# Kernel tuning notes

Measured on AMD Instinct MI355X. Metric: run time of the kernel, lower is better.

The kernel has to match this reference:

```python
import jax, jax.numpy as jnp
from jax import lax
import numpy as np

SIGMA = 0.4        # guided-attention diagonal width
PAD_MAG = 1e12     # -inf surrogate used by the torch viterbi


def _viterbi_align(logp, text_lens, mel_lens):
    """Monotonic forced alignment. logp: (B, L, T). Returns hard alignment (B, L, T)."""
    B, L, T = logp.shape
    neg = jnp.asarray(-PAD_MAG, logp.dtype)
    # ---- forward DP over time (lax.scan replaces the python loop over T) ----
    init = jnp.full((B, L), neg, logp.dtype).at[:, 0].set(logp[:, 0, 0])
    lp_T = jnp.moveaxis(logp, 2, 0)  # (T, B, L)

    def fwd(prev, lp_t):
        # transition: stay at same text token, or advance by one (shift down along L)
        shifted = jnp.concatenate([jnp.full((B, 1), neg, logp.dtype), prev[:, :-1]], axis=1)
        cur = jnp.maximum(prev, shifted) + lp_t
        return cur, cur

    _, betas = lax.scan(fwd, init, lp_T[1:])
    log_beta = jnp.concatenate([init[None], betas], axis=0)  # (T, B, L), indexed [t, b, l]

    # ---- backtracking (faithful to the float row/col arithmetic in the source) ----
    barange = jnp.arange(B)
    rows0 = (text_lens - 1).astype(logp.dtype)
    cols0 = (mel_lens - 1).astype(logp.dtype)

    def bwd(carry, _):
        rows, cols = carry
        r = rows.astype(jnp.int32)
        c = cols.astype(jnp.int32)
        cm1 = (c - 1) % T  # torch negative indexing wraps; emulate with mod
        g_go = log_beta[cm1, barange, (r - 1) % L]
        g_stay = log_beta[cm1, barange, r % L]
        is_go = (g_go > g_stay).astype(logp.dtype)
        new_rows = jnp.maximum(rows - is_go + 1.0, 0.0) - 1.0  # relu(x)-1 as in source
        new_cols = jnp.maximum(cols, 0.0) - 1.0
        return (new_rows, new_cols), new_rows

    _, rows_seq = lax.scan(bwd, (rows0, cols0), None, length=T - 1)  # r_1 .. r_{T-1}
    path = jnp.concatenate([rows_seq[::-1], rows0[None]], axis=0).T  # (B, T)

    # one-hot over text positions (static width L instead of path.max()+1)
    align = (path[:, :, None] == jnp.arange(L, dtype=path.dtype)[None, None, :]).astype(logp.dtype)  # (B,T,L)

    # per-batch shift: drop first (T - mel_len) frames, zero-pad at the end
    pad = T - mel_lens  # (B,)
    t_idx = jnp.arange(T)[None, :] + pad[:, None]  # (B, T)
    valid = (t_idx < T)
    gathered = jnp.take_along_axis(align, jnp.clip(t_idx, 0, T - 1)[:, :, None], axis=1)
    align = gathered * valid[:, :, None].astype(logp.dtype)
    return jnp.swapaxes(align, 1, 2)  # (B, L, T)


def _guided_attention_loss(att_ws, ilens, olens, sigma=SIGMA):
    """att_ws: (B, T_out, T_in). Masked guided-attention loss (scalar)."""
    B, T, L = att_ws.shape
    t = jnp.arange(T, dtype=att_ws.dtype)[None, :, None]
    l = jnp.arange(L, dtype=att_ws.dtype)[None, None, :]
    il = ilens.astype(att_ws.dtype)[:, None, None]
    ol = olens.astype(att_ws.dtype)[:, None, None]
    w = 1.0 - jnp.exp(-((l / il - t / ol) ** 2) / (2.0 * sigma * sigma))
    valid = (t < ol) & (l < il)
    return jnp.sum(jnp.where(valid, w * att_ws, 0.0)) / jnp.sum(olens).astype(att_ws.dtype)


def setup_inputs() -> dict:
    key = jax.random.key(0)
    k1, k2, k3, k4 = jax.random.split(key, 4)
    B, L, T = 32, 256, 2048
    log_prob_matrix = jax.nn.log_softmax(jax.random.normal(k1, (B, L, T), jnp.float32), axis=1)
    att_ws = jax.nn.softmax(jax.random.normal(k2, (B, T, L), jnp.float32), axis=-1)
    text_lengths = jax.random.randint(k3, (B,), L // 2, L + 1, dtype=jnp.int32)
    mel_lengths = jax.random.randint(k4, (B,), T // 2, T + 1, dtype=jnp.int32)
    return {
        "log_prob_matrix": log_prob_matrix,
        "att_ws": att_ws,
        "text_lengths": text_lengths,
        "mel_lengths": mel_lengths,
    }


def reference(log_prob_matrix, att_ws, text_lengths, mel_lengths):
    # n_frames_per_step = 1 -> olens = mel_lengths (clamped to att width T, trivially true)
    loss = _guided_attention_loss(att_ws, text_lengths, mel_lengths)
    align = _viterbi_align(log_prob_matrix, text_lengths, mel_lengths)
    return loss, align
```

## Files before the change

### kernel.cpp

```cpp
#include <hip/hip_runtime.h>
#include <cstdint>

#define NEG (-1e12f)
constexpr int Bn = 32, Ln = 256, Tn = 2048;
constexpr int TB = Tn / 64;


__device__ inline float dpp_ror1(float x) {
    int xi = __float_as_int(x);
    return __int_as_float(__builtin_amdgcn_update_dpp(xi, xi, 0x13C, 0xF, 0xF, false));
}

__device__ inline uint32_t lds_off(const void* p) {
    return (uint32_t)(uintptr_t)(__attribute__((address_space(3))) const void*)p;
}

#define BARRIER() { asm volatile("" ::: "memory"); \
                    __builtin_amdgcn_s_barrier(); \
                    asm volatile("" ::: "memory"); }

#define DSRX(DST, ROW, BUF) \
    asm volatile("ds_read_b128 %0, %1 offset:%c2" \
        : "=&v"(DST) \
        : "v"((((ROW) >> 2) & 1) ? vxb : vxa), \
          "i"((BUF) * 16384 + ((ROW) & 15) * 1024));

#define W4 { asm volatile("s_waitcnt lgkmcnt(4)"); __builtin_amdgcn_sched_barrier(0); }

#define ABIT(ACC, X, Y) \
    asm("v_cmp_gt_f32 vcc, %1, %2\n\tv_addc_co_u32 %0, vcc, %0, %0, vcc" \
        : "+v"(ACC) : "v"(X), "v"(Y) : "vcc");

#define STEPS(S, Q) { \
    if ((((S) - 1) & 32) == 0) { ABIT(a0hi, svp, pv0) } else { ABIT(a0lo, svp, pv0) } \
    float c3 = fmaxf(pv3, pv2) + (Q).w; \
    float sv = dpp_ror1(c3); \
    float c2 = fmaxf(pv2, pv1) + (Q).z; \
    float c1 = fmaxf(pv1, pv0) + (Q).y; \
    float lf = isl0 ? negc : svp; \
    float c0 = fmaxf(pv0, lf) + (Q).x; \
    if (((S) & 32) == 0) { \
        ABIT(a1hi, c0, c1) ABIT(a2hi, c1, c2) ABIT(a3hi, c2, c3) \
    } else { \
        ABIT(a1lo, c0, c1) ABIT(a2lo, c1, c2) ABIT(a3lo, c2, c3) \
    } \
    if ((S) == 63) { \
        bb[(size_t)(4 * lane + 1) * TB + m] = ((uint64_t)a1hi << 32) | a1lo; \
        bb[(size_t)(4 * lane + 2) * TB + m] = ((uint64_t)a2hi << 32) | a2lo; \
        bb[(size_t)(4 * lane + 3) * TB + m] = ((uint64_t)a3hi << 32) | a3lo; \
        a1lo = a1hi = a2lo = a2hi = a3lo = a3hi = 0; \
    } \
    if ((S) == 64) { \
        bb[(size_t)(4 * lane + 0) * TB + m] = ((uint64_t)a0hi << 32) | a0lo; \
        a0lo = a0hi = 0; \
    } \
    pv0 = c0; pv1 = c1; pv2 = c2; pv3 = c3; svp = sv; }

#define COMP16X(I) { \
    W4 \
    STEPS(16*(I)+ 1, qq0) STEPS(16*(I)+ 2, qq1) STEPS(16*(I)+ 3, qq2) STEPS(16*(I)+ 4, qq3) \
    DSRX(qq0,  9, (I)) DSRX(qq1, 10, (I)) DSRX(qq2, 11, (I)) DSRX(qq3, 12, (I)) \
    W4 \
    STEPS(16*(I)+ 5, qq4) STEPS(16*(I)+ 6, qq5) STEPS(16*(I)+ 7, qq6) STEPS(16*(I)+ 8, qq7) \
    DSRX(qq4, 13, (I)) DSRX(qq5, 14, (I)) DSRX(qq6, 15, (I)) DSRX(qq7,  0, ((I)+1)&3) \
    W4 \
    STEPS(16*(I)+ 9, qq0) STEPS(16*(I)+10, qq1) STEPS(16*(I)+11, qq2) STEPS(16*(I)+12, qq3) \
    DSRX(qq0,  1, ((I)+1)&3) DSRX(qq1,  2, ((I)+1)&3) DSRX(qq2,  3, ((I)+1)&3) DSRX(qq3,  4, ((I)+1)&3) \
    W4 \
    STEPS(16*(I)+13, qq4) STEPS(16*(I)+14, qq5) STEPS(16*(I)+15, qq6) STEPS(16*(I)+16, qq7) \
    DSRX(qq4,  5, ((I)+1)&3) DSRX(qq5,  6, ((I)+1)&3) DSRX(qq6,  7, ((I)+1)&3) DSRX(qq7,  8, ((I)+1)&3) \
    BARRIER() }

#define PLOAD(P) { \
    xh0 = *(const float4*)(pr0 + 16 * (P)); \
    xh1 = *(const float4*)(pr1 + 16 * (P)); \
    xh2 = *(const float4*)(pr2 + 16 * (P)); \
    xh3 = *(const float4*)(pr3 + 16 * (P)); \
    xh4 = *(const float4*)(pr4 + 16 * (P)); \
    if (six) xh5 = *(const float4*)(pr5 + 16 * (P)); }

#define PW1(XH, CC) { float* rq = rr + (CC); \
    rq[0] = (XH).x; rq[256] = (XH).y; rq[512] = (XH).z; rq[768] = (XH).w; }

#define PWRITE(P) { \
    float* rr = smem + ((P) & 3) * 4096; \
    PW1(xh0, c0) PW1(xh1, c1) PW1(xh2, c2) PW1(xh3, c3) PW1(xh4, c4) \
    if (six) PW1(xh5, c5) }

__global__ void __launch_bounds__(256, 1) k_mega(
        const float* __restrict__ logp, const float* __restrict__ att,
        const int* __restrict__ ilen, const int* __restrict__ olen,
        uint64_t* __restrict__ bits, float* __restrict__ partial) {
    __shared__ __align__(16) float smem[24576];
    int bid = blockIdx.x, tid = threadIdx.x;

    if (bid < 32) {
        int b = bid;
        if (tid < 64) {
            __builtin_amdgcn_s_setprio(1);
            int lane = tid;
            bool isl0 = (lane == 0);
            uint64_t* bb = bits + (size_t)b * (Ln * TB);
            const float negc = NEG;
            uint32_t lb = lds_off(smem) + (uint32_t)(lane * 16);
            uint32_t vxa = lb, vxb = lb ^ 64;

            float pv0, pv1, pv2, pv3, svp;
            uint32_t a0lo = 0, a0hi = 0, a1lo = 0, a1hi = 0;
            uint32_t a2lo = 0, a2hi = 0, a3lo = 0, a3hi = 0;

            {
                float lp00 = logp[(size_t)b * (Ln * Tn)];
                pv0 = isl0 ? lp00 : NEG;
                pv1 = NEG; pv2 = NEG; pv3 = NEG;
                svp = dpp_ror1(pv3);
                a1hi = (pv0 > pv1) ? 1u : 0u;
                a2hi = (pv1 > pv2) ? 1u : 0u;
                a3hi = (pv2 > pv3) ? 1u : 0u;
            }

            BARRIER();
            float4 qq0, qq1, qq2, qq3, qq4, qq5, qq6, qq7;
            DSRX(qq0, 1, 0) DSRX(qq1, 2, 0) DSRX(qq2, 3, 0) DSRX(qq3, 4, 0)
            DSRX(qq4, 5, 0) DSRX(qq5, 6, 0) DSRX(qq6, 7, 0) DSRX(qq7, 8, 0)

            for (int m = 0; m < 32; ++m) {
                COMP16X(0) COMP16X(1) COMP16X(2) COMP16X(3)
            }
            asm volatile("s_waitcnt vmcnt(0)" ::: "memory");
        } else {
            int tid2 = tid - 64;
            bool six = (tid2 < 64);
            const float* lpb = logp + (size_t)b * (Ln * Tn);
            int v0 = tid2, v1 = tid2 + 192, v2 = tid2 + 384,
                v3 = tid2 + 576, v4 = tid2 + 768, v5 = tid2 + 960;
            const float* pr0 = lpb + (size_t)(v0 >> 2) * Tn + 4 * (v0 & 3);
            const float* pr1 = lpb + (size_t)(v1 >> 2) * Tn + 4 * (v1 & 3);
            const float* pr2 = lpb + (size_t)(v2 >> 2) * Tn + 4 * (v2 & 3);
            const float* pr3 = lpb + (size_t)(v3 >> 2) * Tn + 4 * (v3 & 3);
            const float* pr4 = lpb + (size_t)(v4 >> 2) * Tn + 4 * (v4 & 3);
            const float* pr5 = lpb + (size_t)(v5 >> 2) * Tn + 4 * (v5 & 3);
            int c0 = (4 * (v0 & 3)) * 256 + ((v0 >> 2) ^ ((v0 & 1) << 4));
            int c1 = (4 * (v1 & 3)) * 256 + ((v1 >> 2) ^ ((v1 & 1) << 4));
            int c2 = (4 * (v2 & 3)) * 256 + ((v2 >> 2) ^ ((v2 & 1) << 4));
            int c3 = (4 * (v3 & 3)) * 256 + ((v3 >> 2) ^ ((v3 & 1) << 4));
            int c4 = (4 * (v4 & 3)) * 256 + ((v4 >> 2) ^ ((v4 & 1) << 4));
            int c5 = (4 * (v5 & 3)) * 256 + ((v5 >> 2) ^ ((v5 & 1) << 4));
            float4 xh0, xh1, xh2, xh3, xh4, xh5;

            PLOAD(0) PWRITE(0)
            PLOAD(1) PWRITE(1)
            PLOAD(2)
            asm volatile("s_waitcnt lgkmcnt(0)" ::: "memory");
            BARRIER();

            for (int k = 0; k < 128; ++k) {
                if (k <= 125) PWRITE(k + 2)
                if (k <= 124) PLOAD(k + 3)
                asm volatile("s_waitcnt lgkmcnt(0)" ::: "memory");
                BARRIER();
            }
        }
    } else {
        const int N4 = Bn * Tn * Ln / 4;
        int j = bid - 32;
        int idx = j * 256 + tid;
        int stride = 1024 * 256;
        float acc = 0.f;
        for (int v = idx; v < N4; v += stride) {
            int flat = v << 2;
            int b  = flat >> 19;
            int t  = (flat >> 8) & (Tn - 1);
            int l0 = flat & (Ln - 1);
            int ili = ilen[b];
            int oli = olen[b];
            if (t >= oli) continue;
            float il = (float)ili, ol = (float)oli;
            float tf = (float)t / ol;
            float4 a = reinterpret_cast<const float4*>(att)[v];
            #pragma unroll
            for (int c = 0; c < 4; ++c) {
                int l = l0 + c;
                float av = (c == 0) ? a.x : (c == 1) ? a.y : (c == 2) ? a.z : a.w;
                if (l < ili) {
                    float d = (float)l / il - tf;
                    acc += (1.f - __expf(-d * d * 3.125f)) * av;
                }
            }
        }
        for (int off = 32; off > 0; off >>= 1) acc += __shfl_down(acc, off, 64);
        float* sw = smem;
        if ((tid & 63) == 0) sw[tid >> 6] = acc;
        __syncthreads();
        if (tid == 0) partial[j] = (sw[0] + sw[1]) + (sw[2] + sw[3]);
    }
}

__global__ void __launch_bounds__(256) k_backtrack(const uint64_t* __restrict__ bits,
                                                   const int* __restrict__ ilen,
                                                   const int* __restrict__ olen,
                                                   int2* __restrict__ ext) {
    __shared__ uint64_t sb[Ln * TB];
    int b = blockIdx.x, tid = threadIdx.x;
    ext[b * Ln + tid] = make_int2(1, 0);
    const ulonglong2* g = (const ulonglong2*)(bits + (size_t)b * (Ln * TB));
    ulonglong2* s2 = (ulonglong2*)sb;
    #pragma unroll
    for (int i = 0; i < 16; ++i) s2[i * 256 + tid] = g[i * 256 + tid];
    __syncthreads();
    if (tid != 0) return;

    int tl = ilen[b], ml = olen[b];
    int2* eb = ext + b * Ln;
    int r = tl - 1, hi = ml - 1, p = ml - 2;
    if (p < 0) { eb[r] = make_int2(0, hi); return; }
    int c = p >> 6;
    #define LDW(RR) __builtin_bitreverse64(sb[(RR) * TB + c])
    uint64_t w0 = LDW(r);
    uint64_t w1 = LDW(r > 0 ? r - 1 : 0);
    uint64_t w2 = LDW(r > 1 ? r - 2 : 0);
    uint64_t w3 = LDW(r > 2 ? r - 3 : 0);
    int vd = 3;
    while (true) {
        int pb = p & 63;
        uint64_t mask = (pb == 63) ? ~0ull : ((1ull << (pb + 1)) - 1ull);
        uint64_t mm = w0 & mask;
        if (mm == 0) {
            p = (p & ~63) - 1;
            if (p < 0) { eb[r] = make_int2(0, hi); break; }
            c = p >> 6;
            w0 = LDW(r);
            w1 = LDW(r > 0 ? r - 1 : 0);
            w2 = LDW(r > 1 ? r - 2 : 0);
            w3 = LDW(r > 2 ? r - 3 : 0);
            vd = 3;
        } else {
            int q = 63 - __builtin_clzll(mm);
            int tq = (p & ~63) + q;
            eb[r] = make_int2(tq + 1, hi);
            r -= 1;
            if (r < 0) break;
            hi = tq;
            p = tq - 1;
            if (p < 0) { eb[r] = make_int2(0, hi); break; }
            w0 = w1; w1 = w2; w2 = w3; vd -= 1;
            int nc = p >> 6;
            if (nc != c || vd == 0) {
                c = nc;
                w0 = LDW(r);
                w1 = LDW(r > 0 ? r - 1 : 0);
                w2 = LDW(r > 1 ? r - 2 : 0);
                w3 = LDW(r > 2 ? r - 3 : 0);
                vd = 3;
            }
        }
    }
    #undef LDW
}

__global__ void k_fill(const int2* __restrict__ ext, const float* __restrict__ partial,
                       const int* __restrict__ olen, float* __restrict__ out) {
    const int NG = (Bn * Ln * Tn) / 4;
    int idx = blockIdx.x * blockDim.x + threadIdx.x;
    int stride = gridDim.x * blockDim.x;
    for (int i = idx; i < NG; i += stride) {
        if (i == 0) {
            int2 e = ext[0];
            out[1] = (0 >= e.x && 0 <= e.y) ? 1.f : 0.f;
            out[2] = (1 >= e.x && 1 <= e.y) ? 1.f : 0.f;
            out[3] = (2 >= e.x && 2 <= e.y) ? 1.f : 0.f;
            int2 el = ext[Bn * Ln - 1];
            out[(size_t)Bn * Ln * Tn] = (2047 >= el.x && 2047 <= el.y) ? 1.f : 0.f;
            continue;
        }
        int f0 = 4 * i - 1;
        int r0 = f0 >> 11;
        int t0 = f0 & 2047;
        int2 e0 = ext[r0];
        float4 v;
        if (t0 != 2047) {
            v.x = (t0     >= e0.x && t0     <= e0.y) ? 1.f : 0.f;
            v.y = (t0 + 1 >= e0.x && t0 + 1 <= e0.y) ? 1.f : 0.f;
            v.z = (t0 + 2 >= e0.x && t0 + 2 <= e0.y) ? 1.f : 0.f;
            v.w = (t0 + 3 >= e0.x && t0 + 3 <= e0.y) ? 1.f : 0.f;
        } else {
            int2 e1 = ext[r0 + 1];
            v.x = (2047 >= e0.x && 2047 <= e0.y) ? 1.f : 0.f;
            v.y = (0 >= e1.x && 0 <= e1.y) ? 1.f : 0.f;
            v.z = (1 >= e1.x && 1 <= e1.y) ? 1.f : 0.f;
            v.w = (2 >= e1.x && 2 <= e1.y) ? 1.f : 0.f;
        }
        *reinterpret_cast<float4*>(out + (size_t)4 * i) = v;
    }
    if (blockIdx.x == 0) {
        int tid = threadIdx.x;
        float acc = 0.f;
        for (int i = tid; i < 1024; i += 256) acc += partial[i];
        for (int off = 32; off > 0; off >>= 1) acc += __shfl_down(acc, off, 64);
        __shared__ float sw[4];
        if ((tid & 63) == 0) sw[tid >> 6] = acc;
        __syncthreads();
        if (tid == 0) {
            float tot = (sw[0] + sw[1]) + (sw[2] + sw[3]);
            int so = 0;
            for (int i = 0; i < Bn; ++i) so += olen[i];
            out[0] = tot / (float)so;
        }
    }
}

extern "C" void kernel_launch(void* const* d_in, const int* in_sizes, int n_in,
                              void* d_out, int out_size, void* d_ws, size_t ws_size,
                              hipStream_t stream) {
    const float* logp = (const float*)d_in[0];
    const float* att  = (const float*)d_in[1];
    const int* tlen   = (const int*)d_in[2];
    const int* mlen   = (const int*)d_in[3];
    float* out = (float*)d_out;
    uint64_t* bits = (uint64_t*)d_ws;
    float* partial = (float*)((char*)d_ws + 2097152);
    int2* ext = (int2*)((char*)d_ws + 2101248);

    k_mega<<<32 + 1024, 256, 0, stream>>>(logp, att, tlen, mlen, bits, partial);
    k_backtrack<<<Bn, 256, 0, stream>>>(bits, tlen, mlen, ext);
    k_fill<<<2048, 256, 0, stream>>>(ext, partial, mlen, out);
}
```

Before: 135.5 us.

## Zero output in mega kernel, fuse backtrack with sparse one-hot fill

The output is zero-filled by 1024 extra blocks that run concurrently inside the DP/loss mega kernel. The backtrack kernel now keeps its segment extents in LDS and writes only the 1.0 entries of each row, which lets the separate full-output fill kernel and its workspace round-trip be dropped. This is meant to hide the 64MB output write behind the serial Viterbi DP and to remove a launch. The risk is that the zeroing blocks compete for bandwidth with the loss blocks, and the sparse per-row writes are uncoalesced and serialized per thread.

Measured after the change: 130.4 us. 3.7% less time.

```diff
diff --git a/kernel.cpp b/kernel.cpp
--- a/kernel.cpp
+++ b/kernel.cpp
@@ -90,7 +90,8 @@
 __global__ void __launch_bounds__(256, 1) k_mega(
         const float* __restrict__ logp, const float* __restrict__ att,
         const int* __restrict__ ilen, const int* __restrict__ olen,
-        uint64_t* __restrict__ bits, float* __restrict__ partial) {
+        uint64_t* __restrict__ bits, float* __restrict__ partial,
+        float* __restrict__ out) {
     __shared__ __align__(16) float smem[24576];
     int bid = blockIdx.x, tid = threadIdx.x;
 
@@ -161,7 +162,7 @@
                 BARRIER();
             }
         }
-    } else {
+    } else if (bid < 32 + 1024) {
         const int N4 = Bn * Tn * Ln / 4;
         int j = bid - 32;
         int idx = j * 256 + tid;
@@ -193,111 +194,93 @@
         if ((tid & 63) == 0) sw[tid >> 6] = acc;
         __syncthreads();
         if (tid == 0) partial[j] = (sw[0] + sw[1]) + (sw[2] + sw[3]);
+    } else {
+        const int NZ = (Bn * Ln * Tn) / 4;
+        int j = bid - 1056;
+        float4 z = make_float4(0.f, 0.f, 0.f, 0.f);
+        for (int i = j * 256 + tid; i < NZ; i += 1024 * 256)
+            reinterpret_cast<float4*>(out)[i] = z;
+        if (j == 0 && tid == 0) out[(size_t)Bn * Ln * Tn] = 0.f;
     }
 }
 
-__global__ void __launch_bounds__(256) k_backtrack(const uint64_t* __restrict__ bits,
-                                                   const int* __restrict__ ilen,
-                                                   const int* __restrict__ olen,
-                                                   int2* __restrict__ ext) {
+__global__ void __launch_bounds__(256) k_tail(const uint64_t* __restrict__ bits,
+                                              const int* __restrict__ ilen,
+                                              const int* __restrict__ olen,
+                                              const float* __restrict__ partial,
+                                              float* __restrict__ out) {
     __shared__ uint64_t sb[Ln * TB];
+    __shared__ int2 eb[Ln];
+    __shared__ float sw[4];
     int b = blockIdx.x, tid = threadIdx.x;
-    ext[b * Ln + tid] = make_int2(1, 0);
+    eb[tid] = make_int2(1, 0);
     const ulonglong2* g = (const ulonglong2*)(bits + (size_t)b * (Ln * TB));
     ulonglong2* s2 = (ulonglong2*)sb;
     #pragma unroll
     for (int i = 0; i < 16; ++i) s2[i * 256 + tid] = g[i * 256 + tid];
     __syncthreads();
-    if (tid != 0) return;
-
-    int tl = ilen[b], ml = olen[b];
-    int2* eb = ext + b * Ln;
-    int r = tl - 1, hi = ml - 1, p = ml - 2;
-    if (p < 0) { eb[r] = make_int2(0, hi); return; }
-    int c = p >> 6;
-    #define LDW(RR) __builtin_bitreverse64(sb[(RR) * TB + c])
-    uint64_t w0 = LDW(r);
-    uint64_t w1 = LDW(r > 0 ? r - 1 : 0);
-    uint64_t w2 = LDW(r > 1 ? r - 2 : 0);
-    uint64_t w3 = LDW(r > 2 ? r - 3 : 0);
-    int vd = 3;
-    while (true) {
-        int pb = p & 63;
-        uint64_t mask = (pb == 63) ? ~0ull : ((1ull << (pb + 1)) - 1ull);
-        uint64_t mm = w0 & mask;
-        if (mm == 0) {
-            p = (p & ~63) - 1;
-            if (p < 0) { eb[r] = make_int2(0, hi); break; }
-            c = p >> 6;
-            w0 = LDW(r);
-            w1 = LDW(r > 0 ? r - 1 : 0);
-            w2 = LDW(r > 1 ? r - 2 : 0);
-            w3 = LDW(r > 2 ? r - 3 : 0);
-            vd = 3;
-        } else {
-            int q = 63 - __builtin_clzll(mm);
-            int tq = (p & ~63) + q;
-            eb[r] = make_int2(tq + 1, hi);
-            r -= 1;
-            if (r < 0) break;
-            hi = tq;
-            p = tq - 1;
-            if (p < 0) { eb[r] = make_int2(0, hi); break; }
-            w0 = w1; w1 = w2; w2 = w3; vd -= 1;
-            int nc = p >> 6;
-            if (nc != c || vd == 0) {
-                c = nc;
-                w0 = LDW(r);
-                w1 = LDW(r > 0 ? r - 1 : 0);
-                w2 = LDW(r > 1 ? r - 2 : 0);
-                w3 = LDW(r > 2 ? r - 3 : 0);
-                vd = 3;
-            }
+
+    if (tid == 0) {
+        int tl = ilen[b], ml = olen[b];
+        int r = tl - 1, hi = ml - 1, p = ml - 2;
+        if (p < 0) { eb[r] = make_int2(0, hi); }
+        else {
+            int c = p >> 6;
+            #define LDW(RR) __builtin_bitreverse64(sb[(RR) * TB + c])
+            uint64_t w0 = LDW(r);
+            uint64_t w1 = LDW(r > 0 ? r - 1 : 0);
+            uint64_t w2 = LDW(r > 1 ? r - 2 : 0);
+            uint64_t w3 = LDW(r > 2 ? r - 3 : 0);
+            int vd = 3;
+            while (true) {
+                int pb = p & 63;
+                uint64_t mask = (pb == 63) ? ~0ull : ((1ull << (pb + 1)) - 1ull);
+                uint64_t mm = w0 & mask;
+                if (mm == 0) {
+                    p = (p & ~63) - 1;
+                    if (p < 0) { eb[r] = make_int2(0, hi); break; }
+                    c = p >> 6;
+                    w0 = LDW(r);
+                    w1 = LDW(r > 0 ? r - 1 : 0);
+                    w2 = LDW(r > 1 ? r - 2 : 0);
+                    w3 = LDW(r > 2 ? r - 3 : 0);
+                    vd = 3;
+                } else {
+                    int q = 63 - __builtin_clzll(mm);
+                    int tq = (p & ~63) + q;
+                    eb[r] = make_int2(tq + 1, hi);
+                    r -= 1;
+                    if (r < 0) break;
+                    hi = tq;
+                    p = tq - 1;
+                    if (p < 0) { eb[r] = make_int2(0, hi); break; }
+                    w0 = w1; w1 = w2; w2 = w3; vd -= 1;
+                    int nc = p >> 6;
+                    if (nc != c || vd == 0) {
+                        c = nc;
+                        w0 = LDW(r);
+                        w1 = LDW(r > 0 ? r - 1 : 0);
+                        w2 = LDW(r > 1 ? r - 2 : 0);
+                        w3 = LDW(r > 2 ? r - 3 : 0);
+                        vd = 3;
+                    }
+                }
+            }
+            #undef LDW
         }
     }
-    #undef LDW
-}
-
-__global__ void k_fill(const int2* __restrict__ ext, const float* __restrict__ partial,
-                       const int* __restrict__ olen, float* __restrict__ out) {
-    const int NG = (Bn * Ln * Tn) / 4;
-    int idx = blockIdx.x * blockDim.x + threadIdx.x;
-    int stride = gridDim.x * blockDim.x;
-    for (int i = idx; i < NG; i += stride) {
-        if (i == 0) {
-            int2 e = ext[0];
-            out[1] = (0 >= e.x && 0 <= e.y) ? 1.f : 0.f;
-            out[2] = (1 >= e.x && 1 <= e.y) ? 1.f : 0.f;
-            out[3] = (2 >= e.x && 2 <= e.y) ? 1.f : 0.f;
-            int2 el = ext[Bn * Ln - 1];
-            out[(size_t)Bn * Ln * Tn] = (2047 >= el.x && 2047 <= el.y) ? 1.f : 0.f;
-            continue;
-        }
-        int f0 = 4 * i - 1;
-        int r0 = f0 >> 11;
-        int t0 = f0 & 2047;
-        int2 e0 = ext[r0];
-        float4 v;
-        if (t0 != 2047) {
-            v.x = (t0     >= e0.x && t0     <= e0.y) ? 1.f : 0.f;
-            v.y = (t0 + 1 >= e0.x && t0 + 1 <= e0.y) ? 1.f : 0.f;
-            v.z = (t0 + 2 >= e0.x && t0 + 2 <= e0.y) ? 1.f : 0.f;
-            v.w = (t0 + 3 >= e0.x && t0 + 3 <= e0.y) ? 1.f : 0.f;
-        } else {
-            int2 e1 = ext[r0 + 1];
-            v.x = (2047 >= e0.x && 2047 <= e0.y) ? 1.f : 0.f;
-            v.y = (0 >= e1.x && 0 <= e1.y) ? 1.f : 0.f;
-            v.z = (1 >= e1.x && 1 <= e1.y) ? 1.f : 0.f;
-            v.w = (2 >= e1.x && 2 <= e1.y) ? 1.f : 0.f;
-        }
-        *reinterpret_cast<float4*>(out + (size_t)4 * i) = v;
+    __syncthreads();
+
+    {
+        int2 e = eb[tid];
+        float* orow = out + 1 + (((size_t)b * Ln + tid) << 11);
+        for (int t = e.x; t <= e.y; ++t) orow[t] = 1.f;
     }
-    if (blockIdx.x == 0) {
-        int tid = threadIdx.x;
+
+    if (b == 0) {
         float acc = 0.f;
         for (int i = tid; i < 1024; i += 256) acc += partial[i];
         for (int off = 32; off > 0; off >>= 1) acc += __shfl_down(acc, off, 64);
-        __shared__ float sw[4];
         if ((tid & 63) == 0) sw[tid >> 6] = acc;
         __syncthreads();
         if (tid == 0) {
@@ -319,9 +302,8 @@
     float* out = (float*)d_out;
     uint64_t* bits = (uint64_t*)d_ws;
     float* partial = (float*)((char*)d_ws + 2097152);
-    int2* ext = (int2*)((char*)d_ws + 2101248);
-
-    k_mega<<<32 + 1024, 256, 0, stream>>>(logp, att, tlen, mlen, bits, partial);
-    k_backtrack<<<Bn, 256, 0, stream>>>(bits, tlen, mlen, ext);
-    k_fill<<<2048, 256, 0, stream>>>(ext, partial, mlen, out);
-}
+
+    k_mega<<<32 + 1024 + 1024, 256, 0, stream>>>(logp, att, tlen, mlen,
+                                                 bits, partial, out);
+    k_tail<<<Bn, 256, 0, stream>>>(bits, tlen, mlen, partial, out);
+}
```
